# Performance work log

Hardware: AMD Instinct MI355X
Metric: run time of the kernel (lower is better)

Reference implementation:

```python
import jax, jax.numpy as jnp
import numpy as np


def setup_inputs() -> dict:
    key = jax.random.key(0)
    N, E, LENGTH, DIM = 50000, 800000, 128, 128
    k1, k2, k3 = jax.random.split(key, 3)
    x = jax.random.normal(k1, (N, LENGTH), dtype=jnp.float32)
    edge_index = jax.random.randint(k2, (2, E), 0, N, dtype=jnp.int32)
    W = jax.random.normal(k3, (LENGTH, DIM), dtype=jnp.float32) / np.sqrt(LENGTH).astype(np.float32)
    b = jnp.zeros((DIM,), dtype=jnp.float32)
    return {"x": x, "edge_index": edge_index, "W": W, "b": b, "length": LENGTH, "dim": DIM}


def reference(x, edge_index, W, b, length, dim):
    # GCNConv(length, dim) with default add_self_loops + symmetric normalization,
    # then ReLU and softmax over the feature axis (dim=1).
    N = x.shape[0]
    src, dst = edge_index[0], edge_index[1]  # messages flow src -> dst (PyG source_to_target)
    loop = jnp.arange(N, dtype=src.dtype)
    src = jnp.concatenate([src, loop])
    dst = jnp.concatenate([dst, loop])
    # degree (incl. self-loops) computed on destination nodes, as in PyG gcn_norm
    deg = jax.ops.segment_sum(jnp.ones(dst.shape, dtype=x.dtype), dst, num_segments=N)
    dinv = jnp.where(deg > 0, jax.lax.rsqrt(deg), 0.0)
    norm = dinv[src] * dinv[dst]  # [E+N]
    xw = x @ W  # [N, dim] -- transform before propagate (in >= out here)
    msgs = xw[src] * norm[:, None]  # [E+N, dim] gather + scale
    out = jax.ops.segment_sum(msgs, dst, num_segments=N) + b  # scatter-add
    out = jax.nn.relu(out)
    return jax.nn.softmax(out, axis=1)
```

## Files before the change

kernel.cpp:

```cpp
#include <hip/hip_runtime.h>
#include <hip/hip_bf16.h>


#define KDIM 128
#define CAP 48
#define DPAD 16

__device__ __forceinline__ unsigned short f2bf(float f) {
    union { float f; unsigned u; } v; v.f = f;
    unsigned r = v.u + 0x7fff + ((v.u >> 16) & 1);
    return (unsigned short)(r >> 16);
}
__device__ __forceinline__ float bflo(unsigned u) {
    union { unsigned u; float f; } v; v.u = u << 16; return v.f;
}
__device__ __forceinline__ float bfhi(unsigned u) {
    union { unsigned u; float f; } v; v.u = u & 0xffff0000u; return v.f;
}

__global__ __launch_bounds__(256) void fused_k(const float* __restrict__ x,
                                               const float* __restrict__ W,
                                               const int* __restrict__ src,
                                               const int* __restrict__ dst,
                                               int* __restrict__ degi,
                                               unsigned short* __restrict__ csr,
                                               unsigned short* __restrict__ xwh,
                                               int N, int E, int GB) {
    __shared__ float Xl[128 * 17];
    __shared__ float Wl[16 * 132];

    const int tid = threadIdx.x;

    if ((int)blockIdx.x >= GB) {
        int e = ((int)blockIdx.x - GB) * 256 + tid;
        if (e < E) {
            int d = dst[e];
            int s = src[e];
            int pos = atomicAdd(&degi[d * DPAD], 1);
            if (pos < CAP) csr[d * CAP + pos] = (unsigned short)s;
        }
        return;
    }

    const int tx = tid & 15;
    const int ty = tid >> 4;
    const int rbase = (int)blockIdx.x * 128;

    float acc[8][8];
#pragma unroll
    for (int j = 0; j < 8; ++j)
#pragma unroll
        for (int c = 0; c < 8; ++c) acc[j][c] = 0.f;

    for (int kc = 0; kc < KDIM; kc += 16) {
#pragma unroll
        for (int i = 0; i < 2; ++i) {
            int p = tid + 256 * i;
            int row = p >> 2;
            int c4 = p & 3;
            int gr = rbase + row;
            float4 v = make_float4(0.f, 0.f, 0.f, 0.f);
            if (gr < N) v = *(const float4*)(&x[(size_t)gr * KDIM + kc + c4 * 4]);
            float* dp = &Xl[row * 17 + c4 * 4];
            dp[0] = v.x; dp[1] = v.y; dp[2] = v.z; dp[3] = v.w;
        }
#pragma unroll
        for (int i = 0; i < 2; ++i) {
            int p = tid + 256 * i;
            int k = p >> 5;
            int c4 = p & 31;
            float4 v = *(const float4*)(&W[(size_t)(kc + k) * KDIM + c4 * 4]);
            *(float4*)(&Wl[k * 132 + c4 * 4]) = v;
        }
        __syncthreads();

#pragma unroll
        for (int k = 0; k < 16; ++k) {
            float xr[8];
#pragma unroll
            for (int j = 0; j < 8; ++j) xr[j] = Xl[(ty * 8 + j) * 17 + k];
            float4 w0 = *(const float4*)(&Wl[k * 132 + tx * 4]);
            float4 w1 = *(const float4*)(&Wl[k * 132 + tx * 4 + 64]);
#pragma unroll
            for (int j = 0; j < 8; ++j) {
                acc[j][0] += xr[j] * w0.x; acc[j][1] += xr[j] * w0.y;
                acc[j][2] += xr[j] * w0.z; acc[j][3] += xr[j] * w0.w;
                acc[j][4] += xr[j] * w1.x; acc[j][5] += xr[j] * w1.y;
                acc[j][6] += xr[j] * w1.z; acc[j][7] += xr[j] * w1.w;
            }
        }
        __syncthreads();
    }

#pragma unroll
    for (int j = 0; j < 8; ++j) {
        int gr = rbase + ty * 8 + j;
        if (gr < N) {
            ushort4 o0, o1;
            o0.x = f2bf(acc[j][0]); o0.y = f2bf(acc[j][1]);
            o0.z = f2bf(acc[j][2]); o0.w = f2bf(acc[j][3]);
            o1.x = f2bf(acc[j][4]); o1.y = f2bf(acc[j][5]);
            o1.z = f2bf(acc[j][6]); o1.w = f2bf(acc[j][7]);
            *(ushort4*)(&xwh[(size_t)gr * KDIM + tx * 4]) = o0;
            *(ushort4*)(&xwh[(size_t)gr * KDIM + tx * 4 + 64]) = o1;
        }
    }
}

__global__ __launch_bounds__(256) void gather_k(const unsigned short* __restrict__ xwh,
                                                const unsigned short* __restrict__ csr,
                                                const int* __restrict__ degi,
                                                const float* __restrict__ b,
                                                float* __restrict__ out, int N) {
    int node = (blockIdx.x * blockDim.x + threadIdx.x) >> 6;
    if (node >= N) return;
    int lane = threadIdx.x & 63;
    int h = lane >> 4;
    int c = lane & 15;

    int cnt = degi[node * DPAD];
    int ccnt = min(cnt, CAP);
    float dn = rsqrtf((float)(cnt + 1));

    float a[8];
#pragma unroll
    for (int i = 0; i < 8; ++i) a[i] = 0.f;

    if (h == 0) {
        float sn = dn * dn;
        uint4 u = *(const uint4*)(&xwh[(size_t)node * KDIM + c * 8]);
        float4 b0 = *(const float4*)(&b[c * 8]);
        float4 b1 = *(const float4*)(&b[c * 8 + 4]);
        a[0] = bflo(u.x) * sn + b0.x; a[1] = bfhi(u.x) * sn + b0.y;
        a[2] = bflo(u.y) * sn + b0.z; a[3] = bfhi(u.y) * sn + b0.w;
        a[4] = bflo(u.z) * sn + b1.x; a[5] = bfhi(u.z) * sn + b1.y;
        a[6] = bflo(u.w) * sn + b1.z; a[7] = bfhi(u.w) * sn + b1.w;
    }

    int s_l = 0;
    float w_l = 0.f;
    if (lane < ccnt) {
        s_l = csr[(size_t)node * CAP + lane];
        w_l = rsqrtf((float)(degi[s_l * DPAD] + 1));
    }

    int kmax = (ccnt + 3) >> 2;
#pragma unroll 4
    for (int k = 0; k < kmax; ++k) {
        int idx = 4 * k + h;
        int s = __shfl(s_l, idx);
        float nv = __shfl(w_l, idx) * dn;
        uint4 u = *(const uint4*)(&xwh[(size_t)s * KDIM + c * 8]);
        a[0] += bflo(u.x) * nv; a[1] += bfhi(u.x) * nv;
        a[2] += bflo(u.y) * nv; a[3] += bfhi(u.y) * nv;
        a[4] += bflo(u.z) * nv; a[5] += bfhi(u.z) * nv;
        a[6] += bflo(u.w) * nv; a[7] += bfhi(u.w) * nv;
    }

#pragma unroll
    for (int off = 16; off <= 32; off <<= 1) {
#pragma unroll
        for (int i = 0; i < 8; ++i) a[i] += __shfl_xor(a[i], off);
    }

    float mx = -1e30f;
#pragma unroll
    for (int i = 0; i < 8; ++i) {
        a[i] = fmaxf(a[i], 0.f);
        mx = fmaxf(mx, a[i]);
    }
#pragma unroll
    for (int off = 1; off < 16; off <<= 1) mx = fmaxf(mx, __shfl_xor(mx, off));
    float e[8], s = 0.f;
#pragma unroll
    for (int i = 0; i < 8; ++i) {
        e[i] = __expf(a[i] - mx);
        s += e[i];
    }
#pragma unroll
    for (int off = 1; off < 16; off <<= 1) s += __shfl_xor(s, off);
    float rs = 1.0f / s;
    if (h == 0) {
        float4 o0 = make_float4(e[0] * rs, e[1] * rs, e[2] * rs, e[3] * rs);
        float4 o1 = make_float4(e[4] * rs, e[5] * rs, e[6] * rs, e[7] * rs);
        *(float4*)(&out[(size_t)node * KDIM + c * 8]) = o0;
        *(float4*)(&out[(size_t)node * KDIM + c * 8 + 4]) = o1;
    }
}

extern "C" void kernel_launch(void* const* d_in, const int* in_sizes, int n_in,
                              void* d_out, int out_size, void* d_ws, size_t ws_size,
                              hipStream_t stream) {
    const float* x  = (const float*)d_in[0];
    const int*   ei = (const int*)d_in[1];
    const float* W  = (const float*)d_in[2];
    const float* b  = (const float*)d_in[3];

    const int N = in_sizes[0] / KDIM;
    const int E = in_sizes[1] / 2;
    const int* src = ei;
    const int* dst = ei + E;

    unsigned short* xwh  = (unsigned short*)d_ws;
    int*            degi = (int*)(xwh + (size_t)N * KDIM);
    unsigned short* csr  = (unsigned short*)(degi + (size_t)N * DPAD);
    float*          out  = (float*)d_out;

    hipMemsetAsync(degi, 0, (size_t)N * DPAD * sizeof(int), stream);

    const int GB = (N + 127) / 128;
    const int FB = (E + 255) / 256;
    fused_k<<<GB + FB, 256, 0, stream>>>(x, W, src, dst, degi, csr, xwh, N, E, GB);

    gather_k<<<(N + 3) / 4, 256, 0, stream>>>(xwh, csr, degi, b, out, N);
}
```

Before: 169.5 us.

## Split bf16 XW into four column planes and gather 16 neighbors per pass

The GEMM now writes XW as four contiguous 32-column bf16 planes of shape [N,32] instead of row-major [N,128]. The gather kernel walks each plane in turn, with 16 neighbor slots of 4 lanes each, so every pass touches a smaller working set (3.2 MB per plane) that can stay cache-resident. Each neighbor access becomes a 64-byte segment. The aim is better L2/MALL locality for the random row gathers. In exchange, the neighbor list is walked four times, there are more shuffle reductions, and the accumulator registers grow to 32 floats.

Result: slower. 215.9 us (+27.4%).

```diff
diff --git a/kernel.cpp b/kernel.cpp
--- a/kernel.cpp
+++ b/kernel.cpp
@@ -92,6 +92,9 @@
         __syncthreads();
     }
 
+    const size_t N32 = (size_t)N * 32;
+    const int p0 = tx >> 3;
+    const int off = (tx & 7) * 4;
 #pragma unroll
     for (int j = 0; j < 8; ++j) {
         int gr = rbase + ty * 8 + j;
@@ -101,8 +104,8 @@
             o0.z = f2bf(acc[j][2]); o0.w = f2bf(acc[j][3]);
             o1.x = f2bf(acc[j][4]); o1.y = f2bf(acc[j][5]);
             o1.z = f2bf(acc[j][6]); o1.w = f2bf(acc[j][7]);
-            *(ushort4*)(&xwh[(size_t)gr * KDIM + tx * 4]) = o0;
-            *(ushort4*)(&xwh[(size_t)gr * KDIM + tx * 4 + 64]) = o1;
+            *(ushort4*)(&xwh[(size_t)p0 * N32 + (size_t)gr * 32 + off]) = o0;
+            *(ushort4*)(&xwh[(size_t)(p0 + 2) * N32 + (size_t)gr * 32 + off]) = o1;
         }
     }
 }
@@ -115,27 +118,14 @@
     int node = (blockIdx.x * blockDim.x + threadIdx.x) >> 6;
     if (node >= N) return;
     int lane = threadIdx.x & 63;
-    int h = lane >> 4;
-    int c = lane & 15;
+    int slot = lane >> 2;
+    int c = lane & 3;
+
+    const size_t N32 = (size_t)N * 32;
 
     int cnt = degi[node * DPAD];
     int ccnt = min(cnt, CAP);
     float dn = rsqrtf((float)(cnt + 1));
-
-    float a[8];
-#pragma unroll
-    for (int i = 0; i < 8; ++i) a[i] = 0.f;
-
-    if (h == 0) {
-        float sn = dn * dn;
-        uint4 u = *(const uint4*)(&xwh[(size_t)node * KDIM + c * 8]);
-        float4 b0 = *(const float4*)(&b[c * 8]);
-        float4 b1 = *(const float4*)(&b[c * 8 + 4]);
-        a[0] = bflo(u.x) * sn + b0.x; a[1] = bfhi(u.x) * sn + b0.y;
-        a[2] = bflo(u.y) * sn + b0.z; a[3] = bfhi(u.y) * sn + b0.w;
-        a[4] = bflo(u.z) * sn + b1.x; a[5] = bfhi(u.z) * sn + b1.y;
-        a[6] = bflo(u.w) * sn + b1.z; a[7] = bfhi(u.w) * sn + b1.w;
-    }
 
     int s_l = 0;
     float w_l = 0.f;
@@ -144,47 +134,77 @@
         w_l = rsqrtf((float)(degi[s_l * DPAD] + 1));
     }
 
-    int kmax = (ccnt + 3) >> 2;
-#pragma unroll 4
-    for (int k = 0; k < kmax; ++k) {
-        int idx = 4 * k + h;
-        int s = __shfl(s_l, idx);
-        float nv = __shfl(w_l, idx) * dn;
-        uint4 u = *(const uint4*)(&xwh[(size_t)s * KDIM + c * 8]);
-        a[0] += bflo(u.x) * nv; a[1] += bfhi(u.x) * nv;
-        a[2] += bflo(u.y) * nv; a[3] += bfhi(u.y) * nv;
-        a[4] += bflo(u.z) * nv; a[5] += bfhi(u.z) * nv;
-        a[6] += bflo(u.w) * nv; a[7] += bfhi(u.w) * nv;
-    }
-
-#pragma unroll
-    for (int off = 16; off <= 32; off <<= 1) {
-#pragma unroll
-        for (int i = 0; i < 8; ++i) a[i] += __shfl_xor(a[i], off);
+    const int kmax = (ccnt + 15) >> 4;
+    float a[4][8];
+#pragma unroll
+    for (int q = 0; q < 4; ++q)
+#pragma unroll
+        for (int i = 0; i < 8; ++i) a[q][i] = 0.f;
+
+#pragma unroll
+    for (int q = 0; q < 4; ++q) {
+        const unsigned short* plane = xwh + (size_t)q * N32;
+        for (int k = 0; k < kmax; ++k) {
+            int idx = 16 * k + slot;
+            int s = __shfl(s_l, idx);
+            float nv = __shfl(w_l, idx) * dn;
+            uint4 u = *(const uint4*)(&plane[(size_t)s * 32 + c * 8]);
+            a[q][0] += bflo(u.x) * nv; a[q][1] += bfhi(u.x) * nv;
+            a[q][2] += bflo(u.y) * nv; a[q][3] += bfhi(u.y) * nv;
+            a[q][4] += bflo(u.z) * nv; a[q][5] += bfhi(u.z) * nv;
+            a[q][6] += bflo(u.w) * nv; a[q][7] += bfhi(u.w) * nv;
+        }
+        if (slot == 0) {
+            float sn = dn * dn;
+            uint4 u = *(const uint4*)(&plane[(size_t)node * 32 + c * 8]);
+            float4 b0 = *(const float4*)(&b[q * 32 + c * 8]);
+            float4 b1 = *(const float4*)(&b[q * 32 + c * 8 + 4]);
+            a[q][0] += bflo(u.x) * sn + b0.x; a[q][1] += bfhi(u.x) * sn + b0.y;
+            a[q][2] += bflo(u.y) * sn + b0.z; a[q][3] += bfhi(u.y) * sn + b0.w;
+            a[q][4] += bflo(u.z) * sn + b1.x; a[q][5] += bfhi(u.z) * sn + b1.y;
+            a[q][6] += bflo(u.w) * sn + b1.z; a[q][7] += bfhi(u.w) * sn + b1.w;
+        }
+    }
+
+#pragma unroll
+    for (int off = 4; off <= 32; off <<= 1) {
+#pragma unroll
+        for (int q = 0; q < 4; ++q)
+#pragma unroll
+            for (int i = 0; i < 8; ++i) a[q][i] += __shfl_xor(a[q][i], off);
     }
 
     float mx = -1e30f;
 #pragma unroll
-    for (int i = 0; i < 8; ++i) {
-        a[i] = fmaxf(a[i], 0.f);
-        mx = fmaxf(mx, a[i]);
-    }
-#pragma unroll
-    for (int off = 1; off < 16; off <<= 1) mx = fmaxf(mx, __shfl_xor(mx, off));
-    float e[8], s = 0.f;
-#pragma unroll
-    for (int i = 0; i < 8; ++i) {
-        e[i] = __expf(a[i] - mx);
-        s += e[i];
-    }
-#pragma unroll
-    for (int off = 1; off < 16; off <<= 1) s += __shfl_xor(s, off);
+    for (int q = 0; q < 4; ++q)
+#pragma unroll
+        for (int i = 0; i < 8; ++i) {
+            a[q][i] = fmaxf(a[q][i], 0.f);
+            mx = fmaxf(mx, a[q][i]);
+        }
+    mx = fmaxf(mx, __shfl_xor(mx, 1));
+    mx = fmaxf(mx, __shfl_xor(mx, 2));
+
+    float e[4][8], s = 0.f;
+#pragma unroll
+    for (int q = 0; q < 4; ++q)
+#pragma unroll
+        for (int i = 0; i < 8; ++i) {
+            e[q][i] = __expf(a[q][i] - mx);
+            s += e[q][i];
+        }
+    s += __shfl_xor(s, 1);
+    s += __shfl_xor(s, 2);
     float rs = 1.0f / s;
-    if (h == 0) {
-        float4 o0 = make_float4(e[0] * rs, e[1] * rs, e[2] * rs, e[3] * rs);
-        float4 o1 = make_float4(e[4] * rs, e[5] * rs, e[6] * rs, e[7] * rs);
-        *(float4*)(&out[(size_t)node * KDIM + c * 8]) = o0;
-        *(float4*)(&out[(size_t)node * KDIM + c * 8 + 4]) = o1;
+
+    if (slot == 0) {
+#pragma unroll
+        for (int q = 0; q < 4; ++q) {
+            float4 o0 = make_float4(e[q][0] * rs, e[q][1] * rs, e[q][2] * rs, e[q][3] * rs);
+            float4 o1 = make_float4(e[q][4] * rs, e[q][5] * rs, e[q][6] * rs, e[q][7] * rs);
+            *(float4*)(&out[(size_t)node * KDIM + q * 32 + c * 8]) = o0;
+            *(float4*)(&out[(size_t)node * KDIM + q * 32 + c * 8 + 4]) = o1;
+        }
     }
 }
 
```
